# Optimization experiments

Hardware: AMD Instinct MI355X
Metric: run time of the kernel (lower is better)

## Reference

```python
import jax, jax.numpy as jnp
import numpy as np

N = 16384
T = 100          # num_timesteps
THR = 1.0        # spike threshold
TAU = 10.0       # tau_mem
WIDTH = 1.0      # surrogate beta (width_grad)
SCALE = 1.0      # surrogate grad scale (scale_grad)
ALPHA = float(np.exp(-1.0 / TAU))  # membrane decay per step


@jax.custom_vjp
def single_spike(v):
    # SingleSpike: at most one spike per step, heaviside on (v - thr)
    return (v >= THR).astype(v.dtype)

def _ss_fwd(v):
    return single_spike(v), v

def _ss_bwd(v, g):
    # SingleExponential surrogate: scale * exp(-beta * |v - thr|)
    return (g * SCALE * jnp.exp(-WIDTH * jnp.abs(v - THR)),)

single_spike.defvjp(_ss_fwd, _ss_bwd)


def setup_inputs() -> dict:
    key = jax.random.key(0)
    k1, k2 = jax.random.split(key)
    x = jax.random.normal(k1, (N, 2, 4, 4, T), dtype=jnp.float32)
    # SLAYER dense weight: Conv3d kernel [out=1, C=2, H=4, W=4] (no bias)
    W = jax.random.normal(k2, (1, 2, 4, 4), dtype=jnp.float32) * 0.1
    return {"x": x, "W": W}


def reference(x, W):
    # dense projection per timestep: [N,C,H,W,T] x [O,C,H,W] -> [N,O,T]
    weighted = jnp.einsum('nchwt,ochw->not', x, W)
    inp_t = jnp.moveaxis(weighted, -1, 0)  # [T, N, 1]

    def step(v, i):
        # sinabs LIF with norm_input=True: v = alpha*v + (1-alpha)*input
        v = ALPHA * v + (1.0 - ALPHA) * i
        s = single_spike(v)
        return v - s * THR, s  # MembraneSubtract reset

    v0 = jnp.zeros(inp_t.shape[1:], dtype=weighted.dtype)
    _, spikes = jax.lax.scan(step, v0, inp_t)  # spikes: [T, N, 1]
    out = jnp.moveaxis(spikes, 0, -1)          # [N, 1, T]
    return out.reshape(x.shape[0], 1, 1, 1, T)  # match Conv3d output shape
```

## Files before the change

### kernel.cpp

```cpp
#include <hip/hip_runtime.h>


#define T_STEPS 100
#define CHW     32
#define NPB     16
#define PITCH   101

__global__ __launch_bounds__(256, 4)
void exodus_fused(const float* __restrict__ x,
                  const float* __restrict__ W,
                  float* __restrict__ out) {
    __shared__ float s_in[NPB][PITCH];
    __shared__ float s_sp[NPB][PITCH];

    const int tid    = threadIdx.x;
    const int lane   = tid & 63;
    const int wv     = tid >> 6;
    const int n_base = blockIdx.x * NPB;

    float Wr[CHW];
    #pragma unroll
    for (int c = 0; c < CHW; ++c) Wr[c] = W[c];

    if (lane < T_STEPS / 2) {
        for (int i = 0; i < NPB / 4; ++i) {
            const int nl = wv * (NPB / 4) + i;
            const float* xp = x + (size_t)(n_base + nl) * (CHW * T_STEPS) + 2 * lane;
            float a0 = 0.f, a1 = 0.f;
            #pragma unroll
            for (int c = 0; c < CHW; ++c) {
                const float2 v = *reinterpret_cast<const float2*>(xp + c * T_STEPS);
                a0 += Wr[c] * v.x;
                a1 += Wr[c] * v.y;
            }
            s_in[nl][2 * lane]     = a0;
            s_in[nl][2 * lane + 1] = a1;
        }
    }
    __syncthreads();

    if (lane < NPB / 4) {
        const int nl = wv * (NPB / 4) + lane;
        const float A = 0.9048374180359595f;
        const float B = 0.0951625819640404f;
        float v = 0.f;
        #pragma unroll 4
        for (int t = 0; t < T_STEPS; ++t) {
            v = A * v + B * s_in[nl][t];
            const float sp = (v >= 1.0f) ? 1.0f : 0.0f;
            v -= sp;
            s_sp[nl][t] = sp;
        }
    }
    __syncthreads();

    float* op = out + (size_t)n_base * T_STEPS;
    for (int k = tid; k < NPB * T_STEPS; k += 256) {
        op[k] = s_sp[k / T_STEPS][k % T_STEPS];
    }
}

extern "C" void kernel_launch(void* const* d_in, const int* in_sizes, int n_in,
                              void* d_out, int out_size, void* d_ws, size_t ws_size,
                              hipStream_t stream) {
    const float* x = (const float*)d_in[0];
    const float* W = (const float*)d_in[1];
    float* out = (float*)d_out;

    const int N = in_sizes[0] / (CHW * T_STEPS);
    const int grid = N / NPB;
    exodus_fused<<<grid, 256, 0, stream>>>(x, W, out);
}
```

Baseline: 38.66 us.

## Halve neurons per block and double-buffer x loads across channel chunks

Cuts neurons per block from 16 to 8, so there are twice as many blocks and the launch-bounds occupancy hint rises to 8. The projection loop becomes an explicit software pipeline, issuing the next 8-channel group of float2 loads before consuming the current one, to keep more memory requests in flight. Weights are made wave-uniform with readfirstlane, and the membrane update uses fmaf. This adds register pressure from the two load buffers and changes the float rounding of the LIF recurrence, which could flip spikes right at the threshold.

New measurement: 37.64 us. 1.03x faster.

```diff
diff --git a/kernel.cpp b/kernel.cpp
--- a/kernel.cpp
+++ b/kernel.cpp
@@ -3,10 +3,11 @@
 
 #define T_STEPS 100
 #define CHW     32
-#define NPB     16
+#define NPW     2
+#define NPB     8
 #define PITCH   101
 
-__global__ __launch_bounds__(256, 4)
+__global__ __launch_bounds__(256, 8)
 void exodus_fused(const float* __restrict__ x,
                   const float* __restrict__ W,
                   float* __restrict__ out) {
@@ -20,33 +21,62 @@
 
     float Wr[CHW];
     #pragma unroll
-    for (int c = 0; c < CHW; ++c) Wr[c] = W[c];
+    for (int c = 0; c < CHW; ++c)
+        Wr[c] = __int_as_float(__builtin_amdgcn_readfirstlane(__float_as_int(W[c])));
 
     if (lane < T_STEPS / 2) {
-        for (int i = 0; i < NPB / 4; ++i) {
-            const int nl = wv * (NPB / 4) + i;
-            const float* xp = x + (size_t)(n_base + nl) * (CHW * T_STEPS) + 2 * lane;
-            float a0 = 0.f, a1 = 0.f;
-            #pragma unroll
-            for (int c = 0; c < CHW; ++c) {
-                const float2 v = *reinterpret_cast<const float2*>(xp + c * T_STEPS);
-                a0 += Wr[c] * v.x;
-                a1 += Wr[c] * v.y;
-            }
-            s_in[nl][2 * lane]     = a0;
-            s_in[nl][2 * lane + 1] = a1;
+        const float* xw = x + (size_t)(n_base + wv * NPW) * (CHW * T_STEPS) + 2 * lane;
+        const int NSTR = CHW * T_STEPS;
+
+        float2 bA[8], bB[8];
+
+#define ISSUE(buf, base_off)                                                  \
+        _Pragma("unroll")                                                     \
+        for (int j = 0; j < 8; ++j)                                           \
+            buf[j] = *reinterpret_cast<const float2*>(xw + (base_off) + j * T_STEPS);
+
+#define CONSUME(buf, c_off, ax, ay)                                           \
+        _Pragma("unroll")                                                     \
+        for (int j = 0; j < 8; ++j) {                                         \
+            ax = fmaf(Wr[(c_off) + j], buf[j].x, ax);                         \
+            ay = fmaf(Wr[(c_off) + j], buf[j].y, ay);                         \
         }
+
+        float n0x = 0.f, n0y = 0.f, n1x = 0.f, n1y = 0.f;
+
+        ISSUE(bA, 0)
+        ISSUE(bB, 8 * T_STEPS)
+        CONSUME(bA, 0, n0x, n0y)
+        ISSUE(bA, 16 * T_STEPS)
+        CONSUME(bB, 8, n0x, n0y)
+        ISSUE(bB, 24 * T_STEPS)
+        CONSUME(bA, 16, n0x, n0y)
+        ISSUE(bA, NSTR)
+        CONSUME(bB, 24, n0x, n0y)
+        s_in[wv * NPW + 0][2 * lane]     = n0x;
+        s_in[wv * NPW + 0][2 * lane + 1] = n0y;
+        ISSUE(bB, NSTR + 8 * T_STEPS)
+        CONSUME(bA, 0, n1x, n1y)
+        ISSUE(bA, NSTR + 16 * T_STEPS)
+        CONSUME(bB, 8, n1x, n1y)
+        ISSUE(bB, NSTR + 24 * T_STEPS)
+        CONSUME(bA, 16, n1x, n1y)
+        CONSUME(bB, 24, n1x, n1y)
+        s_in[wv * NPW + 1][2 * lane]     = n1x;
+        s_in[wv * NPW + 1][2 * lane + 1] = n1y;
+#undef ISSUE
+#undef CONSUME
     }
     __syncthreads();
 
-    if (lane < NPB / 4) {
-        const int nl = wv * (NPB / 4) + lane;
+    if (lane < NPW) {
+        const int nl = wv * NPW + lane;
         const float A = 0.9048374180359595f;
         const float B = 0.0951625819640404f;
         float v = 0.f;
         #pragma unroll 4
         for (int t = 0; t < T_STEPS; ++t) {
-            v = A * v + B * s_in[nl][t];
+            v = fmaf(A, v, B * s_in[nl][t]);
             const float sp = (v >= 1.0f) ? 1.0f : 0.0f;
             v -= sp;
             s_sp[nl][t] = sp;
```
